# Performance work log

Measured on AMD Instinct MI355X. Metric: run time of the kernel, lower is better.

Reference implementation:

```python
import jax, jax.numpy as jnp
import numpy as np

TAU = 0.5

def _projection(z, W1, b1, W2, b2):
    h = jax.nn.elu(z @ W1.T + b1)
    return h @ W2.T + b2

def _normalize(x, eps=1e-12):
    n = jnp.linalg.norm(x, axis=1, keepdims=True)
    return x / jnp.maximum(n, eps)

def setup_inputs() -> dict:
    key = jax.random.key(0)
    k = jax.random.split(key, 6)
    N, D, P = 8192, 256, 256
    s = 1.0 / np.sqrt(D)
    return {
        "z1": jax.random.normal(k[0], (N, D), jnp.float32),
        "z2": jax.random.normal(k[1], (N, D), jnp.float32),
        "W1": jax.random.normal(k[2], (P, D), jnp.float32) * s,
        "b1": jnp.zeros((P,), jnp.float32),
        "W2": jax.random.normal(k[3], (D, P), jnp.float32) * s,
        "b2": jnp.zeros((D,), jnp.float32),
    }

def reference(z1, z2, W1, b1, W2, b2):
    h1 = _projection(z1, W1, b1, W2, b2)
    h2 = _projection(z2, W1, b1, W2, b2)
    n1 = _normalize(h1)
    n2 = _normalize(h2)
    f11 = jnp.exp((n1 @ n1.T) / TAU)  # [N,N]
    f22 = jnp.exp((n2 @ n2.T) / TAU)
    f12 = jnp.exp((n1 @ n2.T) / TAU)
    d12 = jnp.diagonal(f12)
    l1 = -jnp.log(d12 / (f11.sum(1) + f12.sum(1) - jnp.diagonal(f11)))
    # sim(h2,h1) = f12.T: diag same, row-sum = column-sum of f12
    l2 = -jnp.log(d12 / (f22.sum(1) + f12.sum(0) - jnp.diagonal(f22)))
    return (l1 + l2) * 0.5
```

## Files before the change

### kernel.cpp

```cpp
#include <hip/hip_runtime.h>
#include <hip/hip_bf16.h>
#include <hip/hip_fp8.h>
#include <stdint.h>

#define Nn 8192
#define TWO_N 16384
#define INV_TAU 2.0f
#define EXP2_SCALE 2.885390081777927f

typedef unsigned short u16;
typedef unsigned char u8;
typedef __bf16 bf16x8 __attribute__((ext_vector_type(8)));
typedef float f32x4 __attribute__((ext_vector_type(4)));
typedef int i32x8 __attribute__((ext_vector_type(8)));

typedef const __attribute__((address_space(1))) void* gas_ptr;
typedef __attribute__((address_space(3))) void* las_ptr;

__device__ __forceinline__ void async_copy16(const void* g, void* l) {
  __builtin_amdgcn_global_load_lds((gas_ptr)g, (las_ptr)l, 16, 0, 0);
}

__device__ __forceinline__ float hw_exp2(float x) {
  return __builtin_amdgcn_exp2f(x);
}

__global__ __launch_bounds__(256)
void wcvt(const float* __restrict__ W1, const float* __restrict__ W2,
          __bf16* __restrict__ Wb) {
  int i = (blockIdx.x * 256 + threadIdx.x) * 8;
  const float* s = (i < 65536) ? (W1 + i) : (W2 + (i - 65536));
  float4 a0 = *(const float4*)s, a1 = *(const float4*)(s + 4);
  bf16x8 v = {(__bf16)a0.x, (__bf16)a0.y, (__bf16)a0.z, (__bf16)a0.w,
              (__bf16)a1.x, (__bf16)a1.y, (__bf16)a1.z, (__bf16)a1.w};
  *(bf16x8*)&Wb[i] = v;
}

__global__ __launch_bounds__(256)
void mlp_norm(const float* __restrict__ z1, const float* __restrict__ z2,
              const __bf16* __restrict__ Wb, const float* __restrict__ b1,
              const float* __restrict__ b2,
              u8* __restrict__ Mf8, float* __restrict__ snorm,
              float* __restrict__ rsum) {
  __shared__ __bf16 sZ[64 * 64];
  __shared__ __bf16 sW[256 * 64];
  __shared__ __bf16 sH[64 * 256];
  const int bx = blockIdx.x;
  const int i0 = bx * 64;
  const float* Zsrc = (bx < 128) ? (z1 + (size_t)i0 * 256)
                                 : (z2 + (size_t)(i0 - Nn) * 256);
  const int t = threadIdx.x;
  const int lane = t & 63, wave = t >> 6;
  const int wn = wave * 64;
  const int fr = lane >> 4, fc = lane & 15;
  const int sw = fc & 7;

  const __bf16* Wb1 = Wb;
  const __bf16* Wb2 = Wb + 65536;

  if (t < 64) rsum[i0 + t] = 0.f;

  f32x4 acc[4][4];
#pragma unroll
  for (int a = 0; a < 4; a++)
#pragma unroll
    for (int b = 0; b < 4; b++) acc[a][b] = (f32x4){0.f, 0.f, 0.f, 0.f};

  for (int k0 = 0; k0 < 256; k0 += 64) {
    __syncthreads();
#pragma unroll
    for (int it = 0; it < 8; ++it) {
      int c = t + 256 * it;
      int row = c >> 3, g = (c & 7) ^ (row & 7);
      async_copy16(Wb1 + (size_t)row * 256 + k0 + g * 8, (void*)&sW[c * 8]);
    }
#pragma unroll
    for (int it = 0; it < 2; ++it) {
      int c = t + 256 * it;
      int row = c >> 3, g = (c & 7) ^ (row & 7);
      const float* s = Zsrc + (size_t)row * 256 + k0 + g * 8;
      float4 a0 = *(const float4*)s, a1 = *(const float4*)(s + 4);
      bf16x8 v = {(__bf16)a0.x, (__bf16)a0.y, (__bf16)a0.z, (__bf16)a0.w,
                  (__bf16)a1.x, (__bf16)a1.y, (__bf16)a1.z, (__bf16)a1.w};
      *(bf16x8*)&sZ[c * 8] = v;
    }
    __syncthreads();
#pragma unroll
    for (int ks = 0; ks < 2; ++ks) {
      bf16x8 af[4], bfr[4];
#pragma unroll
      for (int mi = 0; mi < 4; mi++)
        af[mi] = *(const bf16x8*)&sZ[(mi * 16 + fc) * 64 + (((ks * 4 + fr) ^ sw) * 8)];
#pragma unroll
      for (int ni = 0; ni < 4; ni++)
        bfr[ni] = *(const bf16x8*)&sW[(wn + ni * 16 + fc) * 64 + (((ks * 4 + fr) ^ sw) * 8)];
#pragma unroll
      for (int mi = 0; mi < 4; mi++)
#pragma unroll
        for (int ni = 0; ni < 4; ni++)
          acc[mi][ni] = __builtin_amdgcn_mfma_f32_16x16x32_bf16(af[mi], bfr[ni], acc[mi][ni], 0, 0, 0);
    }
  }

  {
    float bv[4];
#pragma unroll
    for (int ni = 0; ni < 4; ni++) bv[ni] = b1[wn + ni * 16 + fc];
#pragma unroll
    for (int mi = 0; mi < 4; mi++)
#pragma unroll
      for (int ni = 0; ni < 4; ni++) {
        int col = wn + ni * 16 + fc;
        int gc = col >> 3;
#pragma unroll
        for (int r = 0; r < 4; r++) {
          int row = mi * 16 + fr * 4 + r;
          float v = acc[mi][ni][r] + bv[ni];
          v = v > 0.f ? v : (__expf(v) - 1.f);
          int pos = (gc & 24) | ((gc & 7) ^ (row & 7));
          sH[row * 256 + pos * 8 + (col & 7)] = (__bf16)v;
          acc[mi][ni][r] = 0.f;
        }
      }
  }

  for (int k0 = 0; k0 < 256; k0 += 64) {
    __syncthreads();
#pragma unroll
    for (int it = 0; it < 8; ++it) {
      int c = t + 256 * it;
      int row = c >> 3, g = (c & 7) ^ (row & 7);
      async_copy16(Wb2 + (size_t)row * 256 + k0 + g * 8, (void*)&sW[c * 8]);
    }
    __syncthreads();
    const int kgb = k0 >> 3;
#pragma unroll
    for (int ks = 0; ks < 2; ++ks) {
      bf16x8 af[4], bfr[4];
#pragma unroll
      for (int mi = 0; mi < 4; mi++)
        af[mi] = *(const bf16x8*)&sH[(mi * 16 + fc) * 256 + (kgb + (((ks * 4 + fr) ^ sw))) * 8];
#pragma unroll
      for (int ni = 0; ni < 4; ni++)
        bfr[ni] = *(const bf16x8*)&sW[(wn + ni * 16 + fc) * 64 + (((ks * 4 + fr) ^ sw) * 8)];
#pragma unroll
      for (int mi = 0; mi < 4; mi++)
#pragma unroll
        for (int ni = 0; ni < 4; ni++)
          acc[mi][ni] = __builtin_amdgcn_mfma_f32_16x16x32_bf16(af[mi], bfr[ni], acc[mi][ni], 0, 0, 0);
    }
  }

  float bv[4];
#pragma unroll
  for (int ni = 0; ni < 4; ni++) bv[ni] = b2[wn + ni * 16 + fc];

  __syncthreads();
  float* red = (float*)sZ;
  float* red2 = red + 256;

#pragma unroll
  for (int mi = 0; mi < 4; mi++) {
    float ssq[4] = {0.f, 0.f, 0.f, 0.f};
#pragma unroll
    for (int ni = 0; ni < 4; ni++)
#pragma unroll
      for (int r = 0; r < 4; r++) {
        float v = acc[mi][ni][r] + bv[ni];
        acc[mi][ni][r] = v;
        ssq[r] += v * v;
      }
#pragma unroll
    for (int r = 0; r < 4; r++) {
      float v = ssq[r];
#pragma unroll
      for (int off = 1; off < 16; off <<= 1) v += __shfl_xor(v, off, 16);
      if (fc == 0) red[(mi * 16 + fr * 4 + r) * 4 + wave] = v;
    }
  }
  __syncthreads();

#pragma unroll
  for (int mi = 0; mi < 4; mi++) {
    float ssq2[4] = {0.f, 0.f, 0.f, 0.f};
#pragma unroll
    for (int r = 0; r < 4; r++) {
      int row = mi * 16 + fr * 4 + r;
      float ss = red[row * 4] + red[row * 4 + 1] + red[row * 4 + 2] + red[row * 4 + 3];
      float rn = 1.f / fmaxf(sqrtf(ss), 1e-12f);
#pragma unroll
      for (int ni = 0; ni < 4; ni++) {
        float v = acc[mi][ni][r] * rn;
        __hip_fp8_e4m3 q(v);
        Mf8[(size_t)(i0 + row) * 256 + wn + ni * 16 + fc] = q.__x;
        float fv = (float)q;
        ssq2[r] += fv * fv;
      }
    }
#pragma unroll
    for (int r = 0; r < 4; r++) {
      float v = ssq2[r];
#pragma unroll
      for (int off = 1; off < 16; off <<= 1) v += __shfl_xor(v, off, 16);
      if (fc == 0) red2[(mi * 16 + fr * 4 + r) * 4 + wave] = v;
    }
  }
  __syncthreads();
  if (t < 64)
    snorm[i0 + t] = red2[t * 4] + red2[t * 4 + 1] + red2[t * 4 + 2] + red2[t * 4 + 3];
}

__global__ __launch_bounds__(256, 2)
void gram_sym(const u8* __restrict__ Mf8, float* __restrict__ rsum) {
  __shared__ u8 sB8[128 * 256];
  const int t = threadIdx.x;
  const int lane = t & 63, wave = t >> 6;
  const int wm = (wave >> 1) * 64, wn = (wave & 1) * 64;
  const int fr = lane >> 4, fc = lane & 15;

  int f = 2111 - blockIdx.x;
  int b = 0;
  while (f >= 2 * (b + 1) * (b + 2)) ++b;
  int rem = f - 2 * b * (b + 1);
  int r = rem / (b + 1);
  int q = rem - r * (b + 1);
  int k = 4 * b + 1 + r;
  const int i_t = 128 - k;
  const int jt0 = i_t + 4 * q;
  const int L = min(4, k - 4 * q);
  const int i0 = i_t * 128;

  i32x8 afr[4][2];
  {
    const u8* Ag = Mf8 + (size_t)i0 * 256;
#pragma unroll
    for (int mi = 0; mi < 4; ++mi) {
      const u8* rp = Ag + (size_t)(wm + mi * 16 + fc) * 256 + fr * 32;
#pragma unroll
      for (int kb = 0; kb < 2; ++kb) {
        int4 lo = *(const int4*)(rp + kb * 128);
        int4 hi = *(const int4*)(rp + kb * 128 + 16);
        afr[mi][kb] = (i32x8){lo.x, lo.y, lo.z, lo.w, hi.x, hi.y, hi.z, hi.w};
      }
    }
  }

  float rowacc[4][4];
  float colps[4][4];
#pragma unroll
  for (int a = 0; a < 4; a++)
#pragma unroll
    for (int rr = 0; rr < 4; rr++) { rowacc[a][rr] = 0.f; colps[a][rr] = 0.f; }

#pragma unroll
  for (int jt = 0; jt < 4; ++jt) {
    if (jt < L) {
      const int j_t = jt0 + jt;

      __syncthreads();

      {
        const u8* Bg = Mf8 + (size_t)j_t * 128 * 256;
#pragma unroll
        for (int it = 0; it < 8; ++it) {
          int c = t + 256 * it;
          int row = c >> 4, slot = c & 15;
          int g = slot ^ (row & 15);
          async_copy16(Bg + (size_t)row * 256 + g * 16, (void*)&sB8[c * 16]);
        }
      }
      __syncthreads();

      f32x4 acc[4][4];
#pragma unroll
      for (int a = 0; a < 4; a++)
#pragma unroll
        for (int bb = 0; bb < 4; bb++) acc[a][bb] = (f32x4){0.f, 0.f, 0.f, 0.f};

#pragma unroll
      for (int kb = 0; kb < 2; ++kb) {
        i32x8 bfrag[4];
#pragma unroll
        for (int ni = 0; ni < 4; ++ni) {
          const u8* base = sB8 + (wn + ni * 16 + fc) * 256;
          int g0 = kb * 8 + fr * 2;
          int4 lo = *(const int4*)(base + ((g0 ^ fc) * 16));
          int4 hi = *(const int4*)(base + (((g0 + 1) ^ fc) * 16));
          bfrag[ni] = (i32x8){lo.x, lo.y, lo.z, lo.w, hi.x, hi.y, hi.z, hi.w};
        }
#pragma unroll
        for (int mi = 0; mi < 4; mi++)
#pragma unroll
          for (int ni = 0; ni < 4; ni++)
            acc[mi][ni] = __builtin_amdgcn_mfma_scale_f32_16x16x128_f8f6f4(
                afr[mi][kb], bfrag[ni], acc[mi][ni], 0, 0, 0, 0x7F, 0, 0x7F);
      }

#pragma unroll
      for (int mi = 0; mi < 4; mi++) {
#pragma unroll
        for (int ni = 0; ni < 4; ni++) {
          float e0 = hw_exp2(acc[mi][ni][0] * EXP2_SCALE);
          float e1 = hw_exp2(acc[mi][ni][1] * EXP2_SCALE);
          float e2 = hw_exp2(acc[mi][ni][2] * EXP2_SCALE);
          float e3 = hw_exp2(acc[mi][ni][3] * EXP2_SCALE);
          rowacc[mi][0] += e0; rowacc[mi][1] += e1;
          rowacc[mi][2] += e2; rowacc[mi][3] += e3;
          colps[jt][ni] += e0 + e1 + e2 + e3;
        }
      }
    }
  }

#pragma unroll
  for (int jt = 0; jt < 4; ++jt) {
    if (jt < L) {
      const int j_t = jt0 + jt;
      if (j_t != i_t) {
        const int j0 = j_t * 128;
#pragma unroll
        for (int ni = 0; ni < 4; ni++) {
          float v = colps[jt][ni];
          v += __shfl_xor(v, 16, 64);
          v += __shfl_xor(v, 32, 64);
          if (fr == 0) atomicAdd(&rsum[j0 + wn + ni * 16 + fc], v);
        }
      }
    }
  }

#pragma unroll
  for (int mi = 0; mi < 4; mi++) {
#pragma unroll
    for (int rr = 0; rr < 4; rr++) {
      float v = rowacc[mi][rr];
#pragma unroll
      for (int off = 1; off < 16; off <<= 1) v += __shfl_xor(v, off, 16);
      rowacc[mi][rr] = v;
    }
  }
  if (fc == 0) {
#pragma unroll
    for (int mi = 0; mi < 4; mi++) {
      int rbase = i0 + wm + mi * 16 + fr * 4;
      atomicAdd(&rsum[rbase + 0], rowacc[mi][0]);
      atomicAdd(&rsum[rbase + 1], rowacc[mi][1]);
      atomicAdd(&rsum[rbase + 2], rowacc[mi][2]);
      atomicAdd(&rsum[rbase + 3], rowacc[mi][3]);
    }
  }
}

__global__ void final_loss(const u8* __restrict__ Mf8, const float* __restrict__ rsum,
                           const float* __restrict__ snorm, float* __restrict__ out) {
  int i = blockIdx.x * 4 + (threadIdx.x >> 6);
  int lane = threadIdx.x & 63;
  unsigned int ua = ((const unsigned int*)(Mf8 + (size_t)i * 256))[lane];
  unsigned int ub = ((const unsigned int*)(Mf8 + (size_t)(Nn + i) * 256))[lane];
  float d = 0.f;
#pragma unroll
  for (int e = 0; e < 4; ++e) {
    __hip_fp8_e4m3 qa, qb;
    qa.__x = (ua >> (8 * e)) & 0xFF;
    qb.__x = (ub >> (8 * e)) & 0xFF;
    d += (float)qa * (float)qb;
  }
#pragma unroll
  for (int off = 32; off; off >>= 1) d += __shfl_xor(d, off, 64);
  if (lane == 0) {
    float den1 = rsum[i] - __expf(snorm[i] * INV_TAU);
    float den2 = rsum[Nn + i] - __expf(snorm[Nn + i] * INV_TAU);
    out[i] = 0.5f * (logf(den1) + logf(den2)) - d * INV_TAU;
  }
}

extern "C" void kernel_launch(void* const* d_in, const int* in_sizes, int n_in,
                              void* d_out, int out_size, void* d_ws, size_t ws_size,
                              hipStream_t stream) {
  const float* z1 = (const float*)d_in[0];
  const float* z2 = (const float*)d_in[1];
  const float* W1 = (const float*)d_in[2];
  const float* b1 = (const float*)d_in[3];
  const float* W2 = (const float*)d_in[4];
  const float* b2 = (const float*)d_in[5];
  float* out = (float*)d_out;

  char* ws = (char*)d_ws;
  u8*     Mf8   = (u8*)(ws);
  float*  rsum  = (float*)(ws + (4u << 20));
  float*  snorm = (float*)(ws + (4u << 20) + 65536);
  __bf16* Wb    = (__bf16*)(ws + (4u << 20) + 131072);

  wcvt<<<64, 256, 0, stream>>>(W1, W2, Wb);

  mlp_norm<<<256, 256, 0, stream>>>(z1, z2, Wb, b1, b2, Mf8, snorm, rsum);

  gram_sym<<<2112, 256, 0, stream>>>(Mf8, rsum);

  final_loss<<<Nn / 4, 256, 0, stream>>>(Mf8, rsum, snorm, out);
}
```

Measured before the change: 172.0 us.

## Double-buffer K-halves of the B tile and raise occupancy in gram_sym

```diff
diff --git a/kernel.cpp b/kernel.cpp
--- a/kernel.cpp
+++ b/kernel.cpp
@@ -210,9 +210,9 @@
     snorm[i0 + t] = red2[t * 4] + red2[t * 4 + 1] + red2[t * 4 + 2] + red2[t * 4 + 3];
 }
 
-__global__ __launch_bounds__(256, 2)
+__global__ __launch_bounds__(256, 3)
 void gram_sym(const u8* __restrict__ Mf8, float* __restrict__ rsum) {
-  __shared__ u8 sB8[128 * 256];
+  __shared__ u8 sB8[2][128 * 128];
   const int t = threadIdx.x;
   const int lane = t & 63, wave = t >> 6;
   const int wm = (wave >> 1) * 64, wn = (wave & 1) * 64;
@@ -230,6 +230,20 @@
   const int L = min(4, k - 4 * q);
   const int i0 = i_t * 128;
 
+#define STAGE_HALF(jtile, h, buf)                                          \
+  {                                                                        \
+    const u8* Bg = Mf8 + (size_t)(jtile) * 128 * 256 + (h) * 128;          \
+    u8* dstb = &sB8[buf][0];                                               \
+    _Pragma("unroll")                                                      \
+    for (int it_ = 0; it_ < 4; ++it_) {                                    \
+      int c_ = t + 256 * it_;                                              \
+      int row_ = c_ >> 3, g_ = (c_ & 7) ^ (row_ & 7);                      \
+      async_copy16(Bg + (size_t)row_ * 256 + g_ * 16, (void*)&dstb[c_ * 16]); \
+    }                                                                      \
+  }
+
+  STAGE_HALF(jt0, 0, 0);
+
   i32x8 afr[4][2];
   {
     const u8* Ag = Mf8 + (size_t)i0 * 256;
@@ -252,40 +266,36 @@
 #pragma unroll
     for (int rr = 0; rr < 4; rr++) { rowacc[a][rr] = 0.f; colps[a][rr] = 0.f; }
 
+  const int xw = fc & 7;
+
 #pragma unroll
   for (int jt = 0; jt < 4; ++jt) {
     if (jt < L) {
       const int j_t = jt0 + jt;
 
-      __syncthreads();
-
-      {
-        const u8* Bg = Mf8 + (size_t)j_t * 128 * 256;
-#pragma unroll
-        for (int it = 0; it < 8; ++it) {
-          int c = t + 256 * it;
-          int row = c >> 4, slot = c & 15;
-          int g = slot ^ (row & 15);
-          async_copy16(Bg + (size_t)row * 256 + g * 16, (void*)&sB8[c * 16]);
+      f32x4 acc[4][4];
+#pragma unroll
+      for (int a = 0; a < 4; a++)
+#pragma unroll
+        for (int bb = 0; bb < 4; bb++) acc[a][bb] = (f32x4){0.f, 0.f, 0.f, 0.f};
+
+#pragma unroll
+      for (int h = 0; h < 2; ++h) {
+        __syncthreads();
+
+        if (h == 0) {
+          STAGE_HALF(j_t, 1, 1);
+        } else if (jt + 1 < L) {
+          STAGE_HALF(j_t + 1, 0, 0);
         }
-      }
-      __syncthreads();
-
-      f32x4 acc[4][4];
-#pragma unroll
-      for (int a = 0; a < 4; a++)
-#pragma unroll
-        for (int bb = 0; bb < 4; bb++) acc[a][bb] = (f32x4){0.f, 0.f, 0.f, 0.f};
-
-#pragma unroll
-      for (int kb = 0; kb < 2; ++kb) {
+
         i32x8 bfrag[4];
 #pragma unroll
         for (int ni = 0; ni < 4; ++ni) {
-          const u8* base = sB8 + (wn + ni * 16 + fc) * 256;
-          int g0 = kb * 8 + fr * 2;
-          int4 lo = *(const int4*)(base + ((g0 ^ fc) * 16));
-          int4 hi = *(const int4*)(base + (((g0 + 1) ^ fc) * 16));
+          const u8* base = &sB8[h][0] + (wn + ni * 16 + fc) * 128;
+          int s0 = fr * 2;
+          int4 lo = *(const int4*)(base + ((s0 ^ xw) * 16));
+          int4 hi = *(const int4*)(base + (((s0 + 1) ^ xw) * 16));
           bfrag[ni] = (i32x8){lo.x, lo.y, lo.z, lo.w, hi.x, hi.y, hi.z, hi.w};
         }
 #pragma unroll
@@ -293,7 +303,7 @@
 #pragma unroll
           for (int ni = 0; ni < 4; ni++)
             acc[mi][ni] = __builtin_amdgcn_mfma_scale_f32_16x16x128_f8f6f4(
-                afr[mi][kb], bfrag[ni], acc[mi][ni], 0, 0, 0, 0x7F, 0, 0x7F);
+                afr[mi][h], bfrag[ni], acc[mi][ni], 0, 0, 0, 0x7F, 0, 0x7F);
       }
 
 #pragma unroll
@@ -311,6 +321,7 @@
       }
     }
   }
+#undef STAGE_HALF
 
 #pragma unroll
   for (int jt = 0; jt < 4; ++jt) {
```

Measured after the change: 233.0 us. 1.35x slower.
